# Kernel tuning notes

Measured on AMD Instinct MI355X. Metric: run time of the kernel, lower is better.

## Reference

```python
import jax, jax.numpy as jnp
import numpy as np

G, N, D = 32, 2048, 128          # graphs, nodes per graph, feature dim
E_PER = 16384                     # edges per graph (avg degree 8)
E = G * E_PER
RATIO = 0.5
K = int(np.ceil(RATIO * N))       # nodes kept per graph = 1024


def setup_inputs() -> dict:
    key = jax.random.key(0)
    ks = jax.random.split(key, 8)
    x = jax.random.normal(ks[0], (G * N, D), dtype=jnp.float32)
    # random intra-graph edges, then offset into the global node index space
    src = jax.random.randint(ks[1], (G, E_PER), 0, N)
    dst = jax.random.randint(ks[2], (G, E_PER), 0, N)
    off = (jnp.arange(G) * N)[:, None]
    edge_index = jnp.stack([(src + off).reshape(-1), (dst + off).reshape(-1)]).astype(jnp.int32)
    batch = jnp.repeat(jnp.arange(G, dtype=jnp.int32), N)
    s = 1.0 / np.sqrt(D)
    w_rel = jax.random.normal(ks[3], (D,), dtype=jnp.float32) * s   # GraphConv lin_rel weight (out=1)
    b_rel = jnp.zeros((), dtype=jnp.float32)                         # GraphConv bias
    w_root = jax.random.normal(ks[4], (D,), dtype=jnp.float32) * s  # GraphConv lin_root (no bias)
    w_lin = jax.random.normal(ks[5], (D,), dtype=jnp.float32) * s   # nn.Linear(in_dim, 1)
    b_lin = jnp.zeros((), dtype=jnp.float32)
    return {"x": x, "edge_index": edge_index, "batch": batch,
            "w_rel": w_rel, "b_rel": b_rel, "w_root": w_root,
            "w_lin": w_lin, "b_lin": b_lin}


def reference(x, edge_index, batch, w_rel, b_rel, w_root, w_lin, b_lin):
    n_nodes = x.shape[0]
    src, dst = edge_index[0], edge_index[1]

    # score1 = GraphConv(x, edge_index): W_root x_i + W_rel * sum_{j->i} x_j + b
    agg = jax.ops.segment_sum(x[src], dst, num_segments=n_nodes)     # [n_nodes, D]
    score1 = agg @ w_rel + b_rel + x @ w_root                         # [n_nodes]
    # score2 = Linear(x)
    score2 = x @ w_lin + b_lin                                        # [n_nodes]
    # elementwise max over the two scores (torch.max over cat dim=1)
    score = jnp.maximum(score1, score2)

    # per-graph topk: batch is block-sorted with equal graph sizes
    _, idx = jax.lax.top_k(score.reshape(G, N), K)                    # [G, K] intra-graph idx
    perm = (idx + (jnp.arange(G) * N)[:, None]).reshape(-1)           # [G*K] global idx

    x_out = x[perm] * jnp.tanh(score[perm])[:, None]                  # [G*K, D]

    # filter_adj: keep edges whose endpoints both survive, re-index nodes.
    # Output edge count is data-dependent; we return a fixed-size reindexed
    # edge_index plus a validity mask (invalid edges set to 0).
    new_idx = jnp.full((n_nodes,), -1, dtype=edge_index.dtype)
    new_idx = new_idx.at[perm].set(jnp.arange(perm.shape[0], dtype=edge_index.dtype))
    ns, nd = new_idx[src], new_idx[dst]
    edge_mask = (ns >= 0) & (nd >= 0)
    new_edge_index = jnp.where(edge_mask, jnp.stack([ns, nd]), 0)

    new_batch = batch[perm]
    return (x_out, new_edge_index, edge_mask, new_batch)
```

## Files before the change

kernel.cpp:

```cpp
#include <hip/hip_runtime.h>
#include <hip/hip_bf16.h>

#define G_     32
#define N_     2048
#define D_     128
#define K_     1024
#define EPER_  16384

__global__ __launch_bounds__(256) void node_dots(
    const float* __restrict__ x,
    const float* __restrict__ w_rel,
    const float* __restrict__ w_root,
    const float* __restrict__ w_lin,
    const float* __restrict__ b_rel_p,
    const float* __restrict__ b_lin_p,
    float* __restrict__ p,
    float* __restrict__ base,
    float* __restrict__ s2,
    int n_nodes)
{
    int wave = (blockIdx.x * 256 + threadIdx.x) >> 6;
    int lane = threadIdx.x & 63;
    int node = wave * 2 + (lane >> 5);
    int c    = lane & 31;
    if (node >= n_nodes) return;

    float4 xv = ((const float4*)(x + (size_t)node * D_))[c];
    float4 wr = ((const float4*)w_rel)[c];
    float4 wo = ((const float4*)w_root)[c];
    float4 wl = ((const float4*)w_lin)[c];

    float pr = xv.x * wr.x + xv.y * wr.y + xv.z * wr.z + xv.w * wr.w;
    float po = xv.x * wo.x + xv.y * wo.y + xv.z * wo.z + xv.w * wo.w;
    float pl = xv.x * wl.x + xv.y * wl.y + xv.z * wl.z + xv.w * wl.w;

    #pragma unroll
    for (int off = 16; off; off >>= 1) {
        pr += __shfl_xor(pr, off);
        po += __shfl_xor(po, off);
        pl += __shfl_xor(pl, off);
    }
    if (c == 0) {
        p[node]    = pr;
        base[node] = po + b_rel_p[0];
        s2[node]   = pl + b_lin_p[0];
    }
}

__global__ __launch_bounds__(1024) void agg_partial(
    const int* __restrict__ src, const int* __restrict__ dst,
    const float* __restrict__ p, float* __restrict__ part)
{
    __shared__ float agg[N_];
    int g = blockIdx.x >> 3;
    int s = blockIdx.x & 7;
    agg[threadIdx.x]        = 0.0f;
    agg[threadIdx.x + 1024] = 0.0f;
    __syncthreads();

    int e0 = g * EPER_ + s * 2048 + threadIdx.x;
    int e1 = e0 + 1024;
    const float* gp = p + (size_t)g * N_;
    atomicAdd(&agg[dst[e0] & (N_ - 1)], gp[src[e0] & (N_ - 1)]);
    atomicAdd(&agg[dst[e1] & (N_ - 1)], gp[src[e1] & (N_ - 1)]);
    __syncthreads();

    float* op = part + ((size_t)g * 8 + s) * N_;
    op[threadIdx.x]        = agg[threadIdx.x];
    op[threadIdx.x + 1024] = agg[threadIdx.x + 1024];
}

__global__ __launch_bounds__(1024) void topk_fused(
    const float* __restrict__ part,
    const float* __restrict__ base, const float* __restrict__ s2,
    float* __restrict__ score,
    int* __restrict__ new_idx, int* __restrict__ perm)
{
    __shared__ unsigned long long keys[N_];
    int g  = blockIdx.x >> 3;
    int ib = blockIdx.x & 7;

    for (int i = threadIdx.x; i < N_; i += 1024) {
        const float* pp = part + (size_t)g * 8 * N_ + i;
        float a = 0.0f;
        #pragma unroll
        for (int s = 0; s < 8; ++s) a += pp[(size_t)s * N_];
        int node = g * N_ + i;
        float sc = fmaxf(base[node] + a, s2[node]);
        if (ib == 0) score[node] = sc;
        unsigned u = __float_as_uint(sc);
        u ^= ((int)u < 0) ? 0xFFFFFFFFu : 0x80000000u;
        keys[i] = ((unsigned long long)u << 32) | (unsigned)(N_ - 1 - i);
    }
    __syncthreads();

    int il = threadIdx.x >> 2;
    int q  = threadIdx.x & 3;
    int i  = ib * 256 + il;
    unsigned long long ki = keys[i];

    const ulonglong2* k2 = (const ulonglong2*)keys + q * 256;
    int c = 0;
    #pragma unroll 8
    for (int j = 0; j < 256; ++j) {
        ulonglong2 kk = k2[(j + q) & 255];
        c += (kk.x > ki) + (kk.y > ki);
    }
    c += __shfl_xor(c, 1);
    c += __shfl_xor(c, 2);
    if (q == 0) {
        int node = g * N_ + i;
        if (c < K_) {
            int pos = g * K_ + c;
            perm[pos] = node;
            new_idx[node] = pos;
        } else {
            new_idx[node] = -1;
        }
    }
}

__global__ __launch_bounds__(256) void gather_edge(
    const float* __restrict__ x, const float* __restrict__ score,
    const int* __restrict__ perm, const int* __restrict__ new_idx,
    const int* __restrict__ src, const int* __restrict__ dst,
    float* __restrict__ out_x, float* __restrict__ out_b,
    float* __restrict__ out_e0, float* __restrict__ out_e1,
    float* __restrict__ out_m, int E)
{
    int b = blockIdx.x;
    if (b < 4096) {
        int t   = b * 256 + threadIdx.x;
        int row = t >> 5;
        int c   = t & 31;
        int node = perm[row];
        float tz = tanhf(score[node]);
        float4 xv = ((const float4*)(x + (size_t)node * D_))[c];
        ((float4*)(out_x + (size_t)row * D_))[c] =
            make_float4(xv.x * tz, xv.y * tz, xv.z * tz, xv.w * tz);
        if (c == 0) out_b[row] = (float)(node >> 11);
    } else {
        int e = (b - 4096) * 256 + threadIdx.x;
        if (e < E) {
            int ns = new_idx[src[e]];
            int nd = new_idx[dst[e]];
            bool m = (ns >= 0) && (nd >= 0);
            out_e0[e] = m ? (float)ns : 0.0f;
            out_e1[e] = m ? (float)nd : 0.0f;
            out_m[e]  = m ? 1.0f : 0.0f;
        }
    }
}

extern "C" void kernel_launch(void* const* d_in, const int* in_sizes, int n_in,
                              void* d_out, int out_size, void* d_ws, size_t ws_size,
                              hipStream_t stream)
{
    const float* x      = (const float*)d_in[0];
    const int*   ei     = (const int*)d_in[1];
    const float* w_rel  = (const float*)d_in[3];
    const float* b_rel  = (const float*)d_in[4];
    const float* w_root = (const float*)d_in[5];
    const float* w_lin  = (const float*)d_in[6];
    const float* b_lin  = (const float*)d_in[7];
    float* out = (float*)d_out;

    const int n_nodes = in_sizes[0] / D_;
    const int E       = in_sizes[1] / 2;
    const int* src = ei;
    const int* dst = ei + E;

    float* p     = (float*)d_ws;
    float* base  = p + n_nodes;
    float* s2    = base + n_nodes;
    float* score = s2 + n_nodes;
    float* part  = score + n_nodes;
    int*   new_idx = (int*)(part + (size_t)G_ * 8 * N_);
    int*   perm    = new_idx + n_nodes;

    const size_t offEI = (size_t)G_ * K_ * D_;
    const size_t offM  = offEI + 2 * (size_t)E;
    const size_t offB  = offM + (size_t)E;

    node_dots<<<n_nodes / 8, 256, 0, stream>>>(
        x, w_rel, w_root, w_lin, b_rel, b_lin, p, base, s2, n_nodes);
    agg_partial<<<G_ * 8, 1024, 0, stream>>>(src, dst, p, part);
    topk_fused<<<G_ * 8, 1024, 0, stream>>>(part, base, s2, score, new_idx, perm);
    gather_edge<<<4096 + 2048, 256, 0, stream>>>(
        x, score, perm, new_idx, src, dst,
        out, out + offB, out + offEI, out + offEI + E, out + offM, E);
}
```

Before: 121.8 us.

## Fuse four pooling kernels into one cooperative kernel with grid syncs

Replaces the four separate launches (node dots, edge aggregation, top-k ranking, gather/edge filter) with a single cooperative kernel of 256 blocks of 1024 threads, using grid.sync between phases. The goal is to remove per-launch overhead and inter-kernel gaps. The top-k rank phase is also restructured so each thread compares four keys against a 64-pair slice and accumulates counts via shared atomics. In exchange, every phase now runs on only 256 blocks, which may reduce parallelism for the memory-bound node-dot and gather phases, and grid-wide barriers add their own cost.

Result: slower. 223.0 us (+83.1%).

```diff
diff --git a/kernel.cpp b/kernel.cpp
--- a/kernel.cpp
+++ b/kernel.cpp
@@ -1,5 +1,7 @@
 #include <hip/hip_runtime.h>
-#include <hip/hip_bf16.h>
+#include <hip/hip_cooperative_groups.h>
+
+namespace cg = cooperative_groups;
 
 #define G_     32
 #define N_     2048
@@ -7,141 +9,152 @@
 #define K_     1024
 #define EPER_  16384
 
-__global__ __launch_bounds__(256) void node_dots(
+__global__ __launch_bounds__(1024) void fused_pool(
     const float* __restrict__ x,
+    const int*   __restrict__ src,
+    const int*   __restrict__ dst,
     const float* __restrict__ w_rel,
+    const float* __restrict__ b_rel_p,
     const float* __restrict__ w_root,
     const float* __restrict__ w_lin,
-    const float* __restrict__ b_rel_p,
     const float* __restrict__ b_lin_p,
     float* __restrict__ p,
     float* __restrict__ base,
     float* __restrict__ s2,
-    int n_nodes)
+    float* __restrict__ score,
+    float* __restrict__ part,
+    int*   __restrict__ new_idx,
+    int*   __restrict__ perm,
+    float* __restrict__ out_x,
+    float* __restrict__ out_b,
+    float* __restrict__ out_e0,
+    float* __restrict__ out_e1,
+    float* __restrict__ out_m)
 {
-    int wave = (blockIdx.x * 256 + threadIdx.x) >> 6;
-    int lane = threadIdx.x & 63;
-    int node = wave * 2 + (lane >> 5);
-    int c    = lane & 31;
-    if (node >= n_nodes) return;
-
-    float4 xv = ((const float4*)(x + (size_t)node * D_))[c];
-    float4 wr = ((const float4*)w_rel)[c];
-    float4 wo = ((const float4*)w_root)[c];
-    float4 wl = ((const float4*)w_lin)[c];
-
-    float pr = xv.x * wr.x + xv.y * wr.y + xv.z * wr.z + xv.w * wr.w;
-    float po = xv.x * wo.x + xv.y * wo.y + xv.z * wo.z + xv.w * wo.w;
-    float pl = xv.x * wl.x + xv.y * wl.y + xv.z * wl.z + xv.w * wl.w;
-
-    #pragma unroll
-    for (int off = 16; off; off >>= 1) {
-        pr += __shfl_xor(pr, off);
-        po += __shfl_xor(po, off);
-        pl += __shfl_xor(pl, off);
-    }
-    if (c == 0) {
-        p[node]    = pr;
-        base[node] = po + b_rel_p[0];
-        s2[node]   = pl + b_lin_p[0];
-    }
-}
-
-__global__ __launch_bounds__(1024) void agg_partial(
-    const int* __restrict__ src, const int* __restrict__ dst,
-    const float* __restrict__ p, float* __restrict__ part)
-{
-    __shared__ float agg[N_];
-    int g = blockIdx.x >> 3;
-    int s = blockIdx.x & 7;
-    agg[threadIdx.x]        = 0.0f;
-    agg[threadIdx.x + 1024] = 0.0f;
-    __syncthreads();
-
-    int e0 = g * EPER_ + s * 2048 + threadIdx.x;
-    int e1 = e0 + 1024;
-    const float* gp = p + (size_t)g * N_;
-    atomicAdd(&agg[dst[e0] & (N_ - 1)], gp[src[e0] & (N_ - 1)]);
-    atomicAdd(&agg[dst[e1] & (N_ - 1)], gp[src[e1] & (N_ - 1)]);
-    __syncthreads();
-
-    float* op = part + ((size_t)g * 8 + s) * N_;
-    op[threadIdx.x]        = agg[threadIdx.x];
-    op[threadIdx.x + 1024] = agg[threadIdx.x + 1024];
-}
-
-__global__ __launch_bounds__(1024) void topk_fused(
-    const float* __restrict__ part,
-    const float* __restrict__ base, const float* __restrict__ s2,
-    float* __restrict__ score,
-    int* __restrict__ new_idx, int* __restrict__ perm)
-{
-    __shared__ unsigned long long keys[N_];
-    int g  = blockIdx.x >> 3;
-    int ib = blockIdx.x & 7;
-
-    for (int i = threadIdx.x; i < N_; i += 1024) {
-        const float* pp = part + (size_t)g * 8 * N_ + i;
-        float a = 0.0f;
+    cg::grid_group grid = cg::this_grid();
+
+    __shared__ unsigned long long keys_s[N_];
+    __shared__ int cnt_s[256];
+
+    const int tid  = threadIdx.x;
+    const int gtid = blockIdx.x * 1024 + tid;
+    const int lane = tid & 63;
+    const int c    = lane & 31;
+
+    {
+        float4 wr = ((const float4*)w_rel)[c];
+        float4 wo = ((const float4*)w_root)[c];
+        float4 wl = ((const float4*)w_lin)[c];
+        float brel = b_rel_p[0], blin = b_lin_p[0];
+        int waveg = gtid >> 6;
         #pragma unroll
-        for (int s = 0; s < 8; ++s) a += pp[(size_t)s * N_];
-        int node = g * N_ + i;
-        float sc = fmaxf(base[node] + a, s2[node]);
-        if (ib == 0) score[node] = sc;
-        unsigned u = __float_as_uint(sc);
-        u ^= ((int)u < 0) ? 0xFFFFFFFFu : 0x80000000u;
-        keys[i] = ((unsigned long long)u << 32) | (unsigned)(N_ - 1 - i);
-    }
-    __syncthreads();
-
-    int il = threadIdx.x >> 2;
-    int q  = threadIdx.x & 3;
-    int i  = ib * 256 + il;
-    unsigned long long ki = keys[i];
-
-    const ulonglong2* k2 = (const ulonglong2*)keys + q * 256;
-    int c = 0;
-    #pragma unroll 8
-    for (int j = 0; j < 256; ++j) {
-        ulonglong2 kk = k2[(j + q) & 255];
-        c += (kk.x > ki) + (kk.y > ki);
-    }
-    c += __shfl_xor(c, 1);
-    c += __shfl_xor(c, 2);
-    if (q == 0) {
-        int node = g * N_ + i;
-        if (c < K_) {
-            int pos = g * K_ + c;
-            perm[pos] = node;
-            new_idx[node] = pos;
-        } else {
-            new_idx[node] = -1;
-        }
-    }
-}
-
-__global__ __launch_bounds__(256) void gather_edge(
-    const float* __restrict__ x, const float* __restrict__ score,
-    const int* __restrict__ perm, const int* __restrict__ new_idx,
-    const int* __restrict__ src, const int* __restrict__ dst,
-    float* __restrict__ out_x, float* __restrict__ out_b,
-    float* __restrict__ out_e0, float* __restrict__ out_e1,
-    float* __restrict__ out_m, int E)
-{
-    int b = blockIdx.x;
-    if (b < 4096) {
-        int t   = b * 256 + threadIdx.x;
-        int row = t >> 5;
-        int c   = t & 31;
-        int node = perm[row];
-        float tz = tanhf(score[node]);
-        float4 xv = ((const float4*)(x + (size_t)node * D_))[c];
-        ((float4*)(out_x + (size_t)row * D_))[c] =
-            make_float4(xv.x * tz, xv.y * tz, xv.z * tz, xv.w * tz);
-        if (c == 0) out_b[row] = (float)(node >> 11);
-    } else {
-        int e = (b - 4096) * 256 + threadIdx.x;
-        if (e < E) {
+        for (int sweep = 0; sweep < 8; ++sweep) {
+            int node = sweep * 8192 + waveg * 2 + (lane >> 5);
+            float4 xv = ((const float4*)(x + (size_t)node * D_))[c];
+            float pr = xv.x * wr.x + xv.y * wr.y + xv.z * wr.z + xv.w * wr.w;
+            float po = xv.x * wo.x + xv.y * wo.y + xv.z * wo.z + xv.w * wo.w;
+            float pl = xv.x * wl.x + xv.y * wl.y + xv.z * wl.z + xv.w * wl.w;
+            #pragma unroll
+            for (int off = 16; off; off >>= 1) {
+                pr += __shfl_xor(pr, off);
+                po += __shfl_xor(po, off);
+                pl += __shfl_xor(pl, off);
+            }
+            if (c == 0) {
+                p[node]    = pr;
+                base[node] = po + brel;
+                s2[node]   = pl + blin;
+            }
+        }
+    }
+    grid.sync();
+
+    const int g  = blockIdx.x >> 3;
+    const int sb = blockIdx.x & 7;
+    {
+        float* agg = (float*)keys_s;
+        agg[tid]        = 0.0f;
+        agg[tid + 1024] = 0.0f;
+        __syncthreads();
+        int e0 = g * EPER_ + sb * 2048 + tid;
+        const float* gp = p + (size_t)g * N_;
+        atomicAdd(&agg[dst[e0] & (N_ - 1)],        gp[src[e0] & (N_ - 1)]);
+        atomicAdd(&agg[dst[e0 + 1024] & (N_ - 1)], gp[src[e0 + 1024] & (N_ - 1)]);
+        __syncthreads();
+        float* op = part + ((size_t)g * 8 + sb) * N_;
+        op[tid]        = agg[tid];
+        op[tid + 1024] = agg[tid + 1024];
+    }
+    grid.sync();
+
+    {
+        for (int i = tid; i < N_; i += 1024) {
+            const float* pp = part + (size_t)g * 8 * N_ + i;
+            float a = 0.0f;
+            #pragma unroll
+            for (int s = 0; s < 8; ++s) a += pp[(size_t)s * N_];
+            int node = g * N_ + i;
+            float sc = fmaxf(base[node] + a, s2[node]);
+            if (sb == 0) score[node] = sc;
+            unsigned u = __float_as_uint(sc);
+            u ^= ((int)u < 0) ? 0xFFFFFFFFu : 0x80000000u;
+            keys_s[i] = ((unsigned long long)u << 32) | (unsigned)(N_ - 1 - i);
+        }
+        if (tid < 256) cnt_s[tid] = 0;
+        __syncthreads();
+
+        int iq = tid & 63;
+        int js = tid >> 6;
+        int ibase = sb * 256 + iq * 4;
+        unsigned long long ki0 = keys_s[ibase + 0];
+        unsigned long long ki1 = keys_s[ibase + 1];
+        unsigned long long ki2 = keys_s[ibase + 2];
+        unsigned long long ki3 = keys_s[ibase + 3];
+        const ulonglong2* k2 = (const ulonglong2*)keys_s + js * 64;
+        int c0 = 0, c1 = 0, c2 = 0, c3 = 0;
+        #pragma unroll 8
+        for (int j = 0; j < 64; ++j) {
+            ulonglong2 kk = k2[j];
+            c0 += (kk.x > ki0) + (kk.y > ki0);
+            c1 += (kk.x > ki1) + (kk.y > ki1);
+            c2 += (kk.x > ki2) + (kk.y > ki2);
+            c3 += (kk.x > ki3) + (kk.y > ki3);
+        }
+        atomicAdd(&cnt_s[iq * 4 + 0], c0);
+        atomicAdd(&cnt_s[iq * 4 + 1], c1);
+        atomicAdd(&cnt_s[iq * 4 + 2], c2);
+        atomicAdd(&cnt_s[iq * 4 + 3], c3);
+        __syncthreads();
+
+        if (tid < 256) {
+            int rank = cnt_s[tid];
+            int node = g * N_ + sb * 256 + tid;
+            if (rank < K_) {
+                int pos = g * K_ + rank;
+                perm[pos] = node;
+                new_idx[node] = pos;
+            } else {
+                new_idx[node] = -1;
+            }
+        }
+    }
+    grid.sync();
+
+    {
+        int rbase = gtid >> 5;
+        #pragma unroll
+        for (int sweep = 0; sweep < 4; ++sweep) {
+            int row  = sweep * 8192 + rbase;
+            int node = perm[row];
+            float tz = tanhf(score[node]);
+            float4 xv = ((const float4*)(x + (size_t)node * D_))[c];
+            ((float4*)(out_x + (size_t)row * D_))[c] =
+                make_float4(xv.x * tz, xv.y * tz, xv.z * tz, xv.w * tz);
+            if (c == 0) out_b[row] = (float)(node >> 11);
+        }
+        #pragma unroll
+        for (int sweep = 0; sweep < 2; ++sweep) {
+            int e = sweep * 262144 + gtid;
             int ns = new_idx[src[e]];
             int nd = new_idx[dst[e]];
             bool m = (ns >= 0) && (nd >= 0);
@@ -182,11 +195,19 @@
     const size_t offM  = offEI + 2 * (size_t)E;
     const size_t offB  = offM + (size_t)E;
 
-    node_dots<<<n_nodes / 8, 256, 0, stream>>>(
-        x, w_rel, w_root, w_lin, b_rel, b_lin, p, base, s2, n_nodes);
-    agg_partial<<<G_ * 8, 1024, 0, stream>>>(src, dst, p, part);
-    topk_fused<<<G_ * 8, 1024, 0, stream>>>(part, base, s2, score, new_idx, perm);
-    gather_edge<<<4096 + 2048, 256, 0, stream>>>(
-        x, score, perm, new_idx, src, dst,
-        out, out + offB, out + offEI, out + offEI + E, out + offM, E);
+    float* out_x  = out;
+    float* out_e0 = out + offEI;
+    float* out_e1 = out + offEI + E;
+    float* out_m  = out + offM;
+    float* out_b  = out + offB;
+
+    void* args[] = {
+        (void*)&x, (void*)&src, (void*)&dst,
+        (void*)&w_rel, (void*)&b_rel, (void*)&w_root, (void*)&w_lin, (void*)&b_lin,
+        (void*)&p, (void*)&base, (void*)&s2, (void*)&score, (void*)&part,
+        (void*)&new_idx, (void*)&perm,
+        (void*)&out_x, (void*)&out_b, (void*)&out_e0, (void*)&out_e1, (void*)&out_m
+    };
+    hipLaunchCooperativeKernel((const void*)fused_pool,
+                               dim3(256), dim3(1024), args, 0, stream);
 }
```
